# Optimization experiments

Hardware: AMD Instinct MI355X
Metric: run time of the kernel (lower is better)

## Reference

```python
import jax, jax.numpy as jnp
import numpy as np

N, L, D = 512, 40, 128      # batch, peptide length, embedding dim
O, K, MHC = 256, 9, 34      # out_channels, kernel_size, mhc_len
STRIDE = 1


def setup_inputs() -> dict:
    key = jax.random.key(0)
    k1, k2, k3 = jax.random.split(key, 3)
    peptide_x = jax.random.normal(k1, (N, L, D), dtype=jnp.float32)
    mhc_x = jax.random.normal(k2, (N, MHC, D), dtype=jnp.float32)
    weight = jax.random.normal(k3, (O, K, MHC), dtype=jnp.float32) * 0.02  # truncated_normal std=0.02 approx
    bias = jnp.zeros((O,), dtype=jnp.float32)
    return {"peptide_x": peptide_x, "mhc_x": mhc_x, "weight": weight, "bias": bias}


def reference(peptide_x, mhc_x, weight, bias):
    # Per-sample dynamic kernel generation: [n, O, d, K]
    kernel = jax.nn.relu(jnp.einsum('nld,okl->nodk', mhc_x, weight))
    k = weight.shape[1]
    T = (peptide_x.shape[1] - k) // STRIDE + 1  # conv1d output length
    # Sliding windows of the peptide: [n, T, K, d]
    idx = jnp.arange(T)[:, None] * STRIDE + jnp.arange(k)[None, :]
    win = peptide_x[:, idx, :]
    # Grouped (groups=batch) conv1d as a batched contraction: [n, O, T]
    out = jnp.einsum('ntkd,nodk->not', win, kernel) + bias[None, :, None]
    return out
```

## Files before the change

### kernel.cpp

```cpp
#include <hip/hip_runtime.h>
#include <hip/hip_bf16.h>

typedef unsigned short u16;
typedef unsigned int u32;
typedef __bf16 bf16x8 __attribute__((ext_vector_type(8)));
typedef float f32x4 __attribute__((ext_vector_type(4)));
typedef unsigned int u32x4 __attribute__((ext_vector_type(4)));
typedef unsigned int u32x2 __attribute__((ext_vector_type(2)));

#define NN 512
#define LL 40
#define DD 128
#define OO 256
#define KK 9
#define MHCL 34
#define TT 32
#define OC 32
#define OCPG 4
#define PSTR 136
#define MSTR 72
#define KSTR 136
#define LPAD 64
#define WPADL 64

#define PEPT_U16 (LL * PSTR)
#define KERN_U16 (32 * KSTR)

__device__ __forceinline__ u16 f2bf(float x) {
    unsigned int u = __builtin_bit_cast(unsigned int, x);
    u = (u + 0x7FFFu + ((u >> 16) & 1u)) >> 16;
    return (u16)u;
}
__device__ __forceinline__ u32 pk2(float a, float b) {
    __hip_bfloat162 h = __float22bfloat162_rn(make_float2(a, b));
    u32 r;
    __builtin_memcpy(&r, &h, 4);
    return r;
}
__device__ __forceinline__ bf16x8 lds_read8(const u16* p) {
    u32x4 r;
    __builtin_memcpy(&r, __builtin_assume_aligned(p, 16), 16);
    return __builtin_bit_cast(bf16x8, r);
}
__device__ __forceinline__ f32x4 mfma16(bf16x8 a, bf16x8 b, f32x4 c) {
    return __builtin_amdgcn_mfma_f32_16x16x32_bf16(a, b, c, 0, 0, 0);
}

__global__ void w_convert(const float* __restrict__ wgt, u32* __restrict__ wp) {
    int i = blockIdx.x * 256 + threadIdx.x;
    if (i >= OO * KK * (WPADL / 2)) return;
    int o = i / (KK * (WPADL / 2));
    int r = i - o * (KK * (WPADL / 2));
    int k = r >> 5;
    int lp = (r & 31) << 1;
    const float* src = wgt + ((size_t)o * KK + k) * MHCL;
    float a = (lp     < MHCL) ? src[lp]     : 0.f;
    float b = (lp + 1 < MHCL) ? src[lp + 1] : 0.f;
    wp[i] = pk2(a, b);
}

template<bool PRE>
__global__ __launch_bounds__(512, 4)
void iconv_kernel(const float* __restrict__ pept,
                  const float* __restrict__ mhc,
                  const float* __restrict__ wgt,
                  const u16* __restrict__ wp,
                  const float* __restrict__ bias,
                  float* __restrict__ out)
{
    __shared__ __align__(16) u16 s_mem[PEPT_U16 + 2 * KERN_U16];

    const int tid  = threadIdx.x;
    const int wave = tid >> 6;
    const int grp  = wave >> 2;
    const int wl   = wave & 3;
    const int lane = tid & 63;
    const int quad = lane >> 4;
    const int l16  = lane & 15;

    const int n = blockIdx.x;

    u16* const s_pept = s_mem;
    u16* const kb     = s_mem + PEPT_U16 + grp * KERN_U16;

    auto loadW = [&](int o_base, int k, bf16x8 wF[2][2]) {
        if (PRE) {
            #pragma unroll
            for (int mt = 0; mt < 2; ++mt) {
                const u16* wr = wp + ((size_t)(o_base + mt * 16 + l16) * KK + k) * WPADL;
                u32x4 r0, r1;
                __builtin_memcpy(&r0, __builtin_assume_aligned(wr + quad * 8, 16), 16);
                __builtin_memcpy(&r1, __builtin_assume_aligned(wr + 32 + quad * 8, 16), 16);
                wF[mt][0] = __builtin_bit_cast(bf16x8, r0);
                wF[mt][1] = __builtin_bit_cast(bf16x8, r1);
            }
        } else {
            #pragma unroll
            for (int mt = 0; mt < 2; ++mt) {
                const float* wrow = wgt + ((size_t)(o_base + mt * 16 + l16) * KK + k) * MHCL;
                float w8[8];
                __builtin_memcpy(w8, __builtin_assume_aligned(wrow + quad * 8, 8), 32);
                u16 h0[8];
                #pragma unroll
                for (int j = 0; j < 8; ++j) h0[j] = f2bf(w8[j]);
                __builtin_memcpy(&wF[mt][0], h0, 16);
                u16 h1[8] = {0,0,0,0,0,0,0,0};
                if (quad == 0) { h1[0] = f2bf(wrow[32]); h1[1] = f2bf(wrow[33]); }
                __builtin_memcpy(&wF[mt][1], h1, 16);
            }
        }
    };

    bf16x8 wFh[2][2];
    loadW((grp * OCPG) * OC, 0, wFh);

    {
        const float* mg = mhc + (size_t)n * MHCL * DD;
        #pragma unroll 1
        for (int i = tid; i < DD * (LPAD / 8); i += 512) {
            int g = i >> 7, d = i & 127;
            u32x4 hh;
            #pragma unroll
            for (int jj = 0; jj < 4; ++jj) {
                int l = g * 8 + jj * 2;
                float a = (l     < MHCL) ? mg[(size_t)l * DD + d]       : 0.f;
                float b = (l + 1 < MHCL) ? mg[(size_t)(l + 1) * DD + d] : 0.f;
                hh[jj] = pk2(a, b);
            }
            __builtin_memcpy(__builtin_assume_aligned(&s_mem[d * MSTR + g * 8], 16), &hh, 16);
        }
    }
    __syncthreads();

    bf16x8 aF[2][2];
    #pragma unroll
    for (int ntl = 0; ntl < 2; ++ntl) {
        const int d = (wl * 2 + ntl) * 16 + l16;
        aF[ntl][0] = lds_read8(&s_mem[d * MSTR + quad * 8]);
        aF[ntl][1] = lds_read8(&s_mem[d * MSTR + 32 + quad * 8]);
    }
    __syncthreads();

    {
        const float* pg = pept + (size_t)n * LL * DD;
        #pragma unroll 1
        for (int i = tid; i < (LL * DD) / 4; i += 512) {
            int row = i >> 5, c4 = (i & 31) << 2;
            f32x4 v;
            __builtin_memcpy(&v, __builtin_assume_aligned(pg + row * DD + c4, 16), 16);
            u32x2 h = { pk2(v[0], v[1]), pk2(v[2], v[3]) };
            __builtin_memcpy(__builtin_assume_aligned(&s_pept[row * PSTR + c4], 8), &h, 8);
        }
    }
    __syncthreads();

    auto stage1 = [&](const bf16x8 wF[2][2]) {
        #pragma unroll
        for (int ntl = 0; ntl < 2; ++ntl) {
            const int nt = wl * 2 + ntl;
            f32x4 c0 = {0.f,0.f,0.f,0.f}, c1 = c0;
            #pragma unroll
            for (int ki = 0; ki < 2; ++ki) {
                c0 = mfma16(aF[ntl][ki], wF[0][ki], c0);
                c1 = mfma16(aF[ntl][ki], wF[1][ki], c1);
            }
            u32x2 p0 = { pk2(fmaxf(c0[0], 0.f), fmaxf(c0[1], 0.f)),
                         pk2(fmaxf(c0[2], 0.f), fmaxf(c0[3], 0.f)) };
            u32x2 p1 = { pk2(fmaxf(c1[0], 0.f), fmaxf(c1[1], 0.f)),
                         pk2(fmaxf(c1[2], 0.f), fmaxf(c1[3], 0.f)) };
            __builtin_memcpy(__builtin_assume_aligned(&kb[l16 * KSTR + nt * 16 + quad * 4], 8), &p0, 8);
            __builtin_memcpy(__builtin_assume_aligned(&kb[(16 + l16) * KSTR + nt * 16 + quad * 4], 8), &p1, 8);
        }
    };

    const int off = wl * 32 + quad * 8;

    #pragma unroll 1
    for (int oci = 0; oci < OCPG; ++oci) {
        const int o_base = (grp * OCPG + oci) * OC;
        f32x4 acc00 = {0.f,0.f,0.f,0.f}, acc01 = acc00, acc10 = acc00, acc11 = acc00;

        stage1(wFh);

        for (int k = 0; k < KK; ++k) {
            bf16x8 wFn[2][2];
            if (k < KK - 1) loadW(o_base, k + 1, wFn);
            bf16x8 bk0 = lds_read8(&kb[l16 * KSTR + off]);
            bf16x8 bk1 = lds_read8(&kb[(16 + l16) * KSTR + off]);
            bf16x8 ap0 = lds_read8(&s_pept[(k + l16) * PSTR + off]);
            bf16x8 ap1 = lds_read8(&s_pept[(k + 16 + l16) * PSTR + off]);
            acc00 = mfma16(ap0, bk0, acc00);
            acc01 = mfma16(ap0, bk1, acc01);
            acc10 = mfma16(ap1, bk0, acc10);
            acc11 = mfma16(ap1, bk1, acc11);
            if (k < KK - 1) stage1(wFn);
        }

        if (oci + 1 < OCPG) loadW((grp * OCPG + oci + 1) * OC, 0, wFh);

        __syncthreads();
        float* red = (float*)kb;
        if (wl < 2) {
            float* rw = red + wl * (TT * 33);
            #pragma unroll
            for (int r = 0; r < 4; ++r) {
                rw[(quad * 4 + r) * 33 + l16]           = acc00[r];
                rw[(quad * 4 + r) * 33 + 16 + l16]      = acc01[r];
                rw[(16 + quad * 4 + r) * 33 + l16]      = acc10[r];
                rw[(16 + quad * 4 + r) * 33 + 16 + l16] = acc11[r];
            }
        }
        __syncthreads();
        if (wl >= 2) {
            float* rw = red + (wl - 2) * (TT * 33);
            #pragma unroll
            for (int r = 0; r < 4; ++r) {
                rw[(quad * 4 + r) * 33 + l16]           += acc00[r];
                rw[(quad * 4 + r) * 33 + 16 + l16]      += acc01[r];
                rw[(16 + quad * 4 + r) * 33 + l16]      += acc10[r];
                rw[(16 + quad * 4 + r) * 33 + 16 + l16] += acc11[r];
            }
        }
        __syncthreads();

        {
            const int lt = tid & 255;
            const int o  = lt >> 3;
            const int t0 = (lt & 7) * 4;
            const float bv = bias[o_base + o];
            f32x4 res;
            #pragma unroll
            for (int j = 0; j < 4; ++j) {
                int idx = (t0 + j) * 33 + o;
                res[j] = red[idx] + red[TT * 33 + idx] + bv;
            }
            float* op = out + ((size_t)n * OO + o_base + o) * TT + t0;
            __builtin_memcpy(__builtin_assume_aligned(op, 16), &res, 16);
        }
        __syncthreads();
    }
}

extern "C" void kernel_launch(void* const* d_in, const int* in_sizes, int n_in,
                              void* d_out, int out_size, void* d_ws, size_t ws_size,
                              hipStream_t stream) {
    const float* pept = (const float*)d_in[0];
    const float* mhc  = (const float*)d_in[1];
    const float* wgt  = (const float*)d_in[2];
    const float* bias = (const float*)d_in[3];
    float* out = (float*)d_out;

    const size_t w_bytes = (size_t)OO * KK * WPADL * sizeof(u16);
    if (ws_size >= w_bytes) {
        w_convert<<<dim3((OO * KK * (WPADL / 2) + 255) / 256), dim3(256), 0, stream>>>(wgt, (u32*)d_ws);
        iconv_kernel<true><<<dim3(NN), dim3(512), 0, stream>>>(pept, mhc, wgt, (const u16*)d_ws, bias, out);
    } else {
        iconv_kernel<false><<<dim3(NN), dim3(512), 0, stream>>>(pept, mhc, wgt, nullptr, bias, out);
    }
}
```

Baseline: 143.9 us.

## Double-buffer per-sample kernel slice in LDS and prefetch weights two steps ahead

The per-sample generated kernel buffer in LDS is split into two halves, so stage1 for k+1 writes one half while the conv MFMAs for k read the other. Weight fragment loads are issued two iterations ahead, and the k loop is fully unrolled. The goal is to overlap kernel generation with the conv contraction and to hide global weight latency. In exchange LDS use grows, which may lower occupancy, and register pressure rises. The code relies on the existing wave-group structure for LDS write/read ordering without adding barriers, which may be a race if waves in a group drift apart.

```diff
diff --git a/kernel.cpp b/kernel.cpp
--- a/kernel.cpp
+++ b/kernel.cpp
@@ -68,7 +68,7 @@
                   const float* __restrict__ bias,
                   float* __restrict__ out)
 {
-    __shared__ __align__(16) u16 s_mem[PEPT_U16 + 2 * KERN_U16];
+    __shared__ __align__(16) u16 s_mem[PEPT_U16 + 4 * KERN_U16];
 
     const int tid  = threadIdx.x;
     const int wave = tid >> 6;
@@ -81,7 +81,7 @@
     const int n = blockIdx.x;
 
     u16* const s_pept = s_mem;
-    u16* const kb     = s_mem + PEPT_U16 + grp * KERN_U16;
+    u16* const kb0    = s_mem + PEPT_U16 + grp * (2 * KERN_U16);
 
     auto loadW = [&](int o_base, int k, bf16x8 wF[2][2]) {
         if (PRE) {
@@ -154,7 +154,8 @@
     }
     __syncthreads();
 
-    auto stage1 = [&](const bf16x8 wF[2][2]) {
+    auto stage1 = [&](const bf16x8 wF[2][2], int buf) {
+        u16* const kbw = kb0 + buf * KERN_U16;
         #pragma unroll
         for (int ntl = 0; ntl < 2; ++ntl) {
             const int nt = wl * 2 + ntl;
@@ -168,8 +169,8 @@
                          pk2(fmaxf(c0[2], 0.f), fmaxf(c0[3], 0.f)) };
             u32x2 p1 = { pk2(fmaxf(c1[0], 0.f), fmaxf(c1[1], 0.f)),
                          pk2(fmaxf(c1[2], 0.f), fmaxf(c1[3], 0.f)) };
-            __builtin_memcpy(__builtin_assume_aligned(&kb[l16 * KSTR + nt * 16 + quad * 4], 8), &p0, 8);
-            __builtin_memcpy(__builtin_assume_aligned(&kb[(16 + l16) * KSTR + nt * 16 + quad * 4], 8), &p1, 8);
+            __builtin_memcpy(__builtin_assume_aligned(&kbw[l16 * KSTR + nt * 16 + quad * 4], 8), &p0, 8);
+            __builtin_memcpy(__builtin_assume_aligned(&kbw[(16 + l16) * KSTR + nt * 16 + quad * 4], 8), &p1, 8);
         }
     };
 
@@ -180,26 +181,36 @@
         const int o_base = (grp * OCPG + oci) * OC;
         f32x4 acc00 = {0.f,0.f,0.f,0.f}, acc01 = acc00, acc10 = acc00, acc11 = acc00;
 
-        stage1(wFh);
-
+        bf16x8 wCur[2][2];
+        loadW(o_base, 1, wCur);
+        stage1(wFh, 0);
+
+        #pragma unroll
         for (int k = 0; k < KK; ++k) {
-            bf16x8 wFn[2][2];
-            if (k < KK - 1) loadW(o_base, k + 1, wFn);
-            bf16x8 bk0 = lds_read8(&kb[l16 * KSTR + off]);
-            bf16x8 bk1 = lds_read8(&kb[(16 + l16) * KSTR + off]);
+            const u16* kbr = kb0 + (k & 1) * KERN_U16;
+            bf16x8 bk0 = lds_read8(&kbr[l16 * KSTR + off]);
+            bf16x8 bk1 = lds_read8(&kbr[(16 + l16) * KSTR + off]);
             bf16x8 ap0 = lds_read8(&s_pept[(k + l16) * PSTR + off]);
             bf16x8 ap1 = lds_read8(&s_pept[(k + 16 + l16) * PSTR + off]);
+            bf16x8 wNext[2][2];
+            if (k + 2 <= KK - 1) loadW(o_base, k + 2, wNext);
+            if (k + 1 <= KK - 1) stage1(wCur, (k + 1) & 1);
             acc00 = mfma16(ap0, bk0, acc00);
             acc01 = mfma16(ap0, bk1, acc01);
             acc10 = mfma16(ap1, bk0, acc10);
             acc11 = mfma16(ap1, bk1, acc11);
-            if (k < KK - 1) stage1(wFn);
+            if (k + 2 <= KK - 1) {
+                #pragma unroll
+                for (int a = 0; a < 2; ++a)
+                    #pragma unroll
+                    for (int b = 0; b < 2; ++b) wCur[a][b] = wNext[a][b];
+            }
         }
 
         if (oci + 1 < OCPG) loadW((grp * OCPG + oci + 1) * OC, 0, wFh);
 
         __syncthreads();
-        float* red = (float*)kb;
+        float* red = (float*)kb0;
         if (wl < 2) {
             float* rw = red + wl * (TT * 33);
             #pragma unroll
```

New measurement: 144.2 us. Within noise of the previous version (+0.2%).
